# Kernel tuning notes

Measured on AMD Instinct MI355X. Metric: run time of the kernel, lower is better.

## Reference

```python
import jax, jax.numpy as jnp
import numpy as np

EPS = 1e-12  # torch F.normalize eps


def setup_inputs() -> dict:
    key = jax.random.key(0)
    ks = jax.random.split(key, 6)
    Bt, St, Bl, Sl, H, D = 128, 256, 128, 32, 768, 128
    return {
        "text_hidden": jax.random.normal(ks[0], (Bt, St, H), dtype=jnp.float32),
        "label_hidden": jax.random.normal(ks[1], (Bl, Sl, H), dtype=jnp.float32),
        "text_mask": jax.random.randint(ks[2], (Bt, St), 0, 2, dtype=jnp.int32),
        "label_mask": jax.random.randint(ks[3], (Bl, Sl), 0, 2, dtype=jnp.int32),
        "targets": jax.random.uniform(ks[4], (Bt, Bl), dtype=jnp.float32),
        "W_proj": jax.random.normal(ks[5], (H, D), dtype=jnp.float32) * (1.0 / np.sqrt(H)),
        "b_proj": jnp.zeros((D,), dtype=jnp.float32),
        "score_scale": jnp.asarray(10.0, dtype=jnp.float32),
    }


def _encode(hidden, W_proj, b_proj):
    # Linear projection + L2 normalize per token (torch F.normalize, eps=1e-12)
    p = hidden @ W_proj + b_proj  # [B, S, D]
    norm = jnp.maximum(jnp.linalg.norm(p, axis=-1, keepdims=True), EPS)
    return p / norm


def _maxsim(text_emb, text_mask, label_emb, label_mask):
    # all-pairs token similarity: [Bt, Bl, St, Sl]
    sim = jnp.einsum("tsd,lrd->tlsr", text_emb, label_emb)
    sim = jnp.where((text_mask == 0)[:, None, :, None], -jnp.inf, sim)
    max_sim = sim.max(axis=2)  # [Bt, Bl, Sl] max over text tokens
    max_sim = jnp.where((label_mask == 0)[None, :, :], 0.0, max_sim)
    label_lengths = jnp.clip(label_mask.sum(axis=-1), 1, None)[None, :]  # [1, Bl]
    return max_sim.sum(axis=-1) / label_lengths.astype(max_sim.dtype)  # [Bt, Bl]


def _bce_with_logits(logits, targets):
    # stable binary_cross_entropy_with_logits, mean reduction
    loss = jnp.maximum(logits, 0.0) - logits * targets + jnp.log1p(jnp.exp(-jnp.abs(logits)))
    return loss.mean()


def reference(text_hidden, label_hidden, text_mask, label_mask, targets, W_proj, b_proj, score_scale):
    text_emb = _encode(text_hidden, W_proj, b_proj)
    label_emb = _encode(label_hidden, W_proj, b_proj)
    logits = score_scale * _maxsim(text_emb, text_mask, label_emb, label_mask)
    loss = _bce_with_logits(logits, targets)
    return loss, jax.nn.sigmoid(logits)
```

## Files before the change

kernel.cpp:

```cpp
#include <hip/hip_runtime.h>
#include <hip/hip_bf16.h>
#include <math.h>

typedef __attribute__((ext_vector_type(8))) short short8;
typedef __attribute__((ext_vector_type(4))) float f32x4;

__device__ inline unsigned short f2bf(float x) {
    union { float f; unsigned u; } v; v.f = x;
    unsigned r = v.u + 0x7fff + ((v.u >> 16) & 1);
    return (unsigned short)(r >> 16);
}
__device__ inline float bf2f(unsigned short h) {
    union { unsigned u; float f; } v; v.u = ((unsigned)h) << 16;
    return v.f;
}

__global__ __launch_bounds__(256) void prep_w_kernel(
    const float* __restrict__ Wm, unsigned short* __restrict__ wfrag)
{
    const int g = blockIdx.x * 256 + threadIdx.x;
    const int c = g >> 10, s = g & 1023;
    const int rem = s & 511;
    const int l = rem & 63;
    const int n = ((rem >> 6) << 4) + (l & 15);
    const int k = c * 64 + ((s >> 9) << 5) + ((l >> 4) << 3);
    short8 hi, lo;
#pragma unroll
    for (int j = 0; j < 8; ++j) {
        const float wv = Wm[(size_t)(k + j) * 128 + n];
        const unsigned short h = f2bf(wv);
        hi[j] = (short)h;
        lo[j] = (short)f2bf(wv - bf2f(h));
    }
    *reinterpret_cast<short8*>(wfrag + (size_t)c * 16384 + s * 8) = hi;
    *reinterpret_cast<short8*>(wfrag + (size_t)c * 16384 + 8192 + s * 8) = lo;
}

__global__ __launch_bounds__(256, 2) void proj_mfma_kernel(
    const float* __restrict__ th, const float* __restrict__ lh,
    const unsigned short* __restrict__ wfrag, const float* __restrict__ bias,
    const int* __restrict__ tmask, const int* __restrict__ lmask,
    unsigned short* __restrict__ emb)
{
    __shared__ short lds[2][16384];
    const int tid = threadIdx.x;
    const int lane = tid & 63, w = tid >> 6;
    const int lq = lane >> 4, lr = lane & 15;
    const int rowg = blockIdx.x * 128;

    const float* sp; const int* mp;
    if (rowg < 32768) { sp = th + (size_t)rowg * 768; mp = tmask + rowg; }
    else { sp = lh + (size_t)(rowg - 32768) * 768; mp = lmask + (rowg - 32768); }

    const float* ap0 = sp + (size_t)(w * 32 + lr) * 768 + lq * 8;
    const float* ap1 = ap0 + (size_t)16 * 768;
    const short* wsrc = reinterpret_cast<const short*>(wfrag);

    f32x4 acc[2][8];
#pragma unroll
    for (int m = 0; m < 2; ++m)
#pragma unroll
        for (int n = 0; n < 8; ++n) acc[m][n] = (f32x4)(0.f);

    float bb[8];
#pragma unroll
    for (int n = 0; n < 8; ++n) bb[n] = bias[n * 16 + lr];

    short8 wst[8];
    f32x4 aA[8];

#pragma unroll
    for (int j = 0; j < 8; ++j)
        wst[j] = *reinterpret_cast<const short8*>(wsrc + (j * 256 + tid) * 8);
#pragma unroll
    for (int j = 0; j < 8; ++j)
        *reinterpret_cast<short8*>(&lds[0][(j * 256 + tid) * 8]) = wst[j];
#pragma unroll
    for (int m = 0; m < 2; ++m)
#pragma unroll
        for (int kcl = 0; kcl < 2; ++kcl)
#pragma unroll
            for (int h = 0; h < 2; ++h)
                aA[m * 4 + kcl * 2 + h] = *reinterpret_cast<const f32x4*>(
                    (m ? ap1 : ap0) + kcl * 32 + h * 4);
#pragma unroll
    for (int j = 0; j < 8; ++j)
        wst[j] = *reinterpret_cast<const short8*>(wsrc + 16384 + (j * 256 + tid) * 8);
    __syncthreads();

    for (int c = 0; c < 12; ++c) {
        const int cb = c & 1;
        short8 ah[2][2], al[2][2];
#pragma unroll
        for (int m = 0; m < 2; ++m)
#pragma unroll
            for (int kcl = 0; kcl < 2; ++kcl) {
                const f32x4 x0 = aA[m * 4 + kcl * 2], x1 = aA[m * 4 + kcl * 2 + 1];
#pragma unroll
                for (int j = 0; j < 8; ++j) {
                    const float av = (j < 4) ? x0[j] : x1[j - 4];
                    const unsigned short h = f2bf(av);
                    ah[m][kcl][j] = (short)h;
                    al[m][kcl][j] = (short)f2bf(av - bf2f(h));
                }
            }
        if (c < 11) {
#pragma unroll
            for (int m = 0; m < 2; ++m)
#pragma unroll
                for (int kcl = 0; kcl < 2; ++kcl)
#pragma unroll
                    for (int h = 0; h < 2; ++h)
                        aA[m * 4 + kcl * 2 + h] = *reinterpret_cast<const f32x4*>(
                            (m ? ap1 : ap0) + (c + 1) * 64 + kcl * 32 + h * 4);
        }
#pragma unroll
        for (int kcl = 0; kcl < 2; ++kcl) {
            short8 wf[8];
#pragma unroll
            for (int n = 0; n < 8; ++n)
                wf[n] = *reinterpret_cast<const short8*>(
                    &lds[cb][kcl * 4096 + n * 512 + lane * 8]);
#pragma unroll
            for (int m = 0; m < 2; ++m)
#pragma unroll
                for (int n = 0; n < 8; ++n)
                    acc[m][n] = __builtin_amdgcn_mfma_f32_16x16x32_bf16(
                        ah[m][kcl], wf[n], acc[m][n], 0, 0, 0);
#pragma unroll
            for (int m = 0; m < 2; ++m)
#pragma unroll
                for (int n = 0; n < 8; ++n)
                    acc[m][n] = __builtin_amdgcn_mfma_f32_16x16x32_bf16(
                        al[m][kcl], wf[n], acc[m][n], 0, 0, 0);
#pragma unroll
            for (int n = 0; n < 8; ++n)
                wf[n] = *reinterpret_cast<const short8*>(
                    &lds[cb][8192 + kcl * 4096 + n * 512 + lane * 8]);
#pragma unroll
            for (int m = 0; m < 2; ++m)
#pragma unroll
                for (int n = 0; n < 8; ++n)
                    acc[m][n] = __builtin_amdgcn_mfma_f32_16x16x32_bf16(
                        ah[m][kcl], wf[n], acc[m][n], 0, 0, 0);
        }
        if (c < 11) {
#pragma unroll
            for (int j = 0; j < 8; ++j)
                *reinterpret_cast<short8*>(&lds[cb ^ 1][(j * 256 + tid) * 8]) = wst[j];
        }
        if (c < 10) {
#pragma unroll
            for (int j = 0; j < 8; ++j)
                wst[j] = *reinterpret_cast<const short8*>(
                    wsrc + (size_t)(c + 2) * 16384 + (j * 256 + tid) * 8);
        }
        __syncthreads();
    }

#pragma unroll
    for (int m = 0; m < 2; ++m) {
#pragma unroll
        for (int n = 0; n < 8; ++n)
#pragma unroll
            for (int i2 = 0; i2 < 4; ++i2) acc[m][n][i2] += bb[n];
        float ss[4];
#pragma unroll
        for (int i2 = 0; i2 < 4; ++i2) {
            float s = 0.f;
#pragma unroll
            for (int n = 0; n < 8; ++n) s += acc[m][n][i2] * acc[m][n][i2];
            s += __shfl_xor(s, 1); s += __shfl_xor(s, 2);
            s += __shfl_xor(s, 4); s += __shfl_xor(s, 8);
            ss[i2] = s;
        }
#pragma unroll
        for (int i2 = 0; i2 < 4; ++i2) {
            const int rowl = w * 32 + m * 16 + lq * 4 + i2;
            float inv = 1.0f / fmaxf(sqrtf(ss[i2]), 1e-12f);
            if (mp[rowl] == 0) inv = 0.f;
#pragma unroll
            for (int n = 0; n < 8; ++n)
                emb[(size_t)(rowg + rowl) * 128 + n * 16 + lr] = f2bf(acc[m][n][i2] * inv);
        }
    }
}

__global__ __launch_bounds__(256, 2) void maxsim_kernel(
    const unsigned short* __restrict__ temb,
    const unsigned short* __restrict__ lemb,
    float* __restrict__ sums)
{
    const int t = blockIdx.x;
    const int bg = blockIdx.y;
    const int tid = threadIdx.x;
    const int lane = tid & 63, w = tid >> 6;
    const int lq = lane >> 4, lr = lane & 15;
    const short* tp = reinterpret_cast<const short*>(temb);
    const short* lp = reinterpret_cast<const short*>(lemb);
    const int l0 = bg * 16 + w * 4;

    short8 bfr[8][4];
#pragma unroll
    for (int n = 0; n < 8; ++n)
#pragma unroll
        for (int kc = 0; kc < 4; ++kc)
            bfr[n][kc] = *reinterpret_cast<const short8*>(
                lp + (size_t)(l0 * 32 + n * 16 + lr) * 128 + kc * 32 + lq * 8);

    f32x4 cmx[8];
#pragma unroll
    for (int n = 0; n < 8; ++n) cmx[n] = (f32x4)(-1e30f);

    const short* ap0 = tp + (size_t)(t * 256 + lr) * 128 + lq * 8;

    for (int m = 0; m < 16; ++m) {
        short8 afr[4];
#pragma unroll
        for (int kc = 0; kc < 4; ++kc)
            afr[kc] = *reinterpret_cast<const short8*>(ap0 + (size_t)m * 16 * 128 + kc * 32);
        f32x4 acc[8];
#pragma unroll
        for (int n = 0; n < 8; ++n) acc[n] = (f32x4)(0.f);
#pragma unroll
        for (int kc = 0; kc < 4; ++kc)
#pragma unroll
            for (int n = 0; n < 8; ++n)
                acc[n] = __builtin_amdgcn_mfma_f32_16x16x32_bf16(afr[kc], bfr[n][kc], acc[n], 0, 0, 0);
#pragma unroll
        for (int n = 0; n < 8; ++n) {
            cmx[n][0] = fmaxf(cmx[n][0], acc[n][0]);
            cmx[n][1] = fmaxf(cmx[n][1], acc[n][1]);
            cmx[n][2] = fmaxf(cmx[n][2], acc[n][2]);
            cmx[n][3] = fmaxf(cmx[n][3], acc[n][3]);
        }
    }

    float s[8];
#pragma unroll
    for (int n = 0; n < 8; ++n) {
        float v = fmaxf(fmaxf(cmx[n][0], cmx[n][1]), fmaxf(cmx[n][2], cmx[n][3]));
        v = fmaxf(v, __shfl_xor(v, 16));
        v = fmaxf(v, __shfl_xor(v, 32));
        v += __shfl_xor(v, 1);
        v += __shfl_xor(v, 2);
        v += __shfl_xor(v, 4);
        v += __shfl_xor(v, 8);
        s[n] = v;
    }
    if (lane == 0) {
#pragma unroll
        for (int li = 0; li < 4; ++li)
            sums[t * 128 + l0 + li] = s[2 * li] + s[2 * li + 1];
    }
}

__global__ __launch_bounds__(256) void finalize_kernel(
    const float* __restrict__ sums, const int* __restrict__ lmask,
    const float* __restrict__ targets, const float* __restrict__ scale_p,
    float* __restrict__ out)
{
    __shared__ float cl[128];
    const int tid = threadIdx.x;
    if (tid < 128) {
        int c = 0;
#pragma unroll
        for (int r = 0; r < 32; ++r) c += lmask[tid * 32 + r];
        cl[tid] = fmaxf((float)c, 1.0f);
    }
    __syncthreads();
    const float scale = *scale_p;
    float sum = 0.f;
    for (int i = tid; i < 16384; i += 256) {
        const float x = scale * sums[i] / cl[i & 127];
        const float tg = targets[i];
        out[1 + i] = 1.0f / (1.0f + expf(-x));
        sum += fmaxf(x, 0.f) - x * tg + log1pf(expf(-fabsf(x)));
    }
    __shared__ float part[4];
#pragma unroll
    for (int msk = 32; msk >= 1; msk >>= 1) sum += __shfl_xor(sum, msk);
    if ((tid & 63) == 0) part[tid >> 6] = sum;
    __syncthreads();
    if (tid == 0)
        out[0] = (part[0] + part[1] + part[2] + part[3]) * (1.0f / 16384.0f);
}

extern "C" void kernel_launch(void* const* d_in, const int* in_sizes, int n_in,
                              void* d_out, int out_size, void* d_ws, size_t ws_size,
                              hipStream_t stream) {
    const float* text_hidden  = (const float*)d_in[0];
    const float* label_hidden = (const float*)d_in[1];
    const int*   text_mask    = (const int*)d_in[2];
    const int*   label_mask   = (const int*)d_in[3];
    const float* targets      = (const float*)d_in[4];
    const float* W_proj       = (const float*)d_in[5];
    const float* b_proj       = (const float*)d_in[6];
    const float* score_scale  = (const float*)d_in[7];
    float* out = (float*)d_out;

    char* ws = (char*)d_ws;
    unsigned short* emb   = (unsigned short*)(ws);
    float*          sums  = (float*)(ws + 9437184);
    unsigned short* wfrag = (unsigned short*)(ws + 9502720);

    prep_w_kernel<<<48, 256, 0, stream>>>(W_proj, wfrag);
    proj_mfma_kernel<<<288, 256, 0, stream>>>(text_hidden, label_hidden, wfrag,
                                              b_proj, text_mask, label_mask, emb);
    maxsim_kernel<<<dim3(128, 8), 256, 0, stream>>>(emb, emb + (size_t)32768 * 128, sums);
    finalize_kernel<<<1, 256, 0, stream>>>(sums, label_mask, targets, score_scale, out);
}
```

Before: 297.9 us.

## Halve projection row tile and parallelize finalize across blocks

The projection kernel now handles 64 rows per block instead of 128, so it launches 576 blocks rather than 288 and spreads the work over more CUs. The cost is that each block reloads all of the W fragments for fewer rows and gets less reuse from its LDS tiles. The single-block finalize becomes a 64-block partial reduction followed by a small one-block sum kernel, which removes the serial loop but adds a kernel launch.

Result: faster. 250.4 us (-15.9%).

```diff
diff --git a/kernel.cpp b/kernel.cpp
--- a/kernel.cpp
+++ b/kernel.cpp
@@ -46,28 +46,25 @@
     const int tid = threadIdx.x;
     const int lane = tid & 63, w = tid >> 6;
     const int lq = lane >> 4, lr = lane & 15;
-    const int rowg = blockIdx.x * 128;
+    const int rowg = blockIdx.x * 64;
 
     const float* sp; const int* mp;
     if (rowg < 32768) { sp = th + (size_t)rowg * 768; mp = tmask + rowg; }
     else { sp = lh + (size_t)(rowg - 32768) * 768; mp = lmask + (rowg - 32768); }
 
-    const float* ap0 = sp + (size_t)(w * 32 + lr) * 768 + lq * 8;
-    const float* ap1 = ap0 + (size_t)16 * 768;
+    const float* ap = sp + (size_t)(w * 16 + lr) * 768 + lq * 8;
     const short* wsrc = reinterpret_cast<const short*>(wfrag);
 
-    f32x4 acc[2][8];
-#pragma unroll
-    for (int m = 0; m < 2; ++m)
-#pragma unroll
-        for (int n = 0; n < 8; ++n) acc[m][n] = (f32x4)(0.f);
+    f32x4 acc[8];
+#pragma unroll
+    for (int n = 0; n < 8; ++n) acc[n] = (f32x4)(0.f);
 
     float bb[8];
 #pragma unroll
     for (int n = 0; n < 8; ++n) bb[n] = bias[n * 16 + lr];
 
     short8 wst[8];
-    f32x4 aA[8];
+    f32x4 aA[4];
 
 #pragma unroll
     for (int j = 0; j < 8; ++j)
@@ -76,13 +73,10 @@
     for (int j = 0; j < 8; ++j)
         *reinterpret_cast<short8*>(&lds[0][(j * 256 + tid) * 8]) = wst[j];
 #pragma unroll
-    for (int m = 0; m < 2; ++m)
-#pragma unroll
-        for (int kcl = 0; kcl < 2; ++kcl)
-#pragma unroll
-            for (int h = 0; h < 2; ++h)
-                aA[m * 4 + kcl * 2 + h] = *reinterpret_cast<const f32x4*>(
-                    (m ? ap1 : ap0) + kcl * 32 + h * 4);
+    for (int kcl = 0; kcl < 2; ++kcl)
+#pragma unroll
+        for (int h = 0; h < 2; ++h)
+            aA[kcl * 2 + h] = *reinterpret_cast<const f32x4*>(ap + kcl * 32 + h * 4);
 #pragma unroll
     for (int j = 0; j < 8; ++j)
         wst[j] = *reinterpret_cast<const short8*>(wsrc + 16384 + (j * 256 + tid) * 8);
@@ -90,29 +84,25 @@
 
     for (int c = 0; c < 12; ++c) {
         const int cb = c & 1;
-        short8 ah[2][2], al[2][2];
-#pragma unroll
-        for (int m = 0; m < 2; ++m)
-#pragma unroll
-            for (int kcl = 0; kcl < 2; ++kcl) {
-                const f32x4 x0 = aA[m * 4 + kcl * 2], x1 = aA[m * 4 + kcl * 2 + 1];
-#pragma unroll
-                for (int j = 0; j < 8; ++j) {
-                    const float av = (j < 4) ? x0[j] : x1[j - 4];
-                    const unsigned short h = f2bf(av);
-                    ah[m][kcl][j] = (short)h;
-                    al[m][kcl][j] = (short)f2bf(av - bf2f(h));
-                }
+        short8 ah[2], al[2];
+#pragma unroll
+        for (int kcl = 0; kcl < 2; ++kcl) {
+            const f32x4 x0 = aA[kcl * 2], x1 = aA[kcl * 2 + 1];
+#pragma unroll
+            for (int j = 0; j < 8; ++j) {
+                const float av = (j < 4) ? x0[j] : x1[j - 4];
+                const unsigned short h = f2bf(av);
+                ah[kcl][j] = (short)h;
+                al[kcl][j] = (short)f2bf(av - bf2f(h));
             }
+        }
         if (c < 11) {
 #pragma unroll
-            for (int m = 0; m < 2; ++m)
-#pragma unroll
-                for (int kcl = 0; kcl < 2; ++kcl)
-#pragma unroll
-                    for (int h = 0; h < 2; ++h)
-                        aA[m * 4 + kcl * 2 + h] = *reinterpret_cast<const f32x4*>(
-                            (m ? ap1 : ap0) + (c + 1) * 64 + kcl * 32 + h * 4);
+            for (int kcl = 0; kcl < 2; ++kcl)
+#pragma unroll
+                for (int h = 0; h < 2; ++h)
+                    aA[kcl * 2 + h] = *reinterpret_cast<const f32x4*>(
+                        ap + (c + 1) * 64 + kcl * 32 + h * 4);
         }
 #pragma unroll
         for (int kcl = 0; kcl < 2; ++kcl) {
@@ -122,27 +112,18 @@
                 wf[n] = *reinterpret_cast<const short8*>(
                     &lds[cb][kcl * 4096 + n * 512 + lane * 8]);
 #pragma unroll
-            for (int m = 0; m < 2; ++m)
-#pragma unroll
-                for (int n = 0; n < 8; ++n)
-                    acc[m][n] = __builtin_amdgcn_mfma_f32_16x16x32_bf16(
-                        ah[m][kcl], wf[n], acc[m][n], 0, 0, 0);
-#pragma unroll
-            for (int m = 0; m < 2; ++m)
-#pragma unroll
-                for (int n = 0; n < 8; ++n)
-                    acc[m][n] = __builtin_amdgcn_mfma_f32_16x16x32_bf16(
-                        al[m][kcl], wf[n], acc[m][n], 0, 0, 0);
+            for (int n = 0; n < 8; ++n)
+                acc[n] = __builtin_amdgcn_mfma_f32_16x16x32_bf16(ah[kcl], wf[n], acc[n], 0, 0, 0);
+#pragma unroll
+            for (int n = 0; n < 8; ++n)
+                acc[n] = __builtin_amdgcn_mfma_f32_16x16x32_bf16(al[kcl], wf[n], acc[n], 0, 0, 0);
 #pragma unroll
             for (int n = 0; n < 8; ++n)
                 wf[n] = *reinterpret_cast<const short8*>(
                     &lds[cb][8192 + kcl * 4096 + n * 512 + lane * 8]);
 #pragma unroll
-            for (int m = 0; m < 2; ++m)
-#pragma unroll
-                for (int n = 0; n < 8; ++n)
-                    acc[m][n] = __builtin_amdgcn_mfma_f32_16x16x32_bf16(
-                        ah[m][kcl], wf[n], acc[m][n], 0, 0, 0);
+            for (int n = 0; n < 8; ++n)
+                acc[n] = __builtin_amdgcn_mfma_f32_16x16x32_bf16(ah[kcl], wf[n], acc[n], 0, 0, 0);
         }
         if (c < 11) {
 #pragma unroll
@@ -159,30 +140,27 @@
     }
 
 #pragma unroll
-    for (int m = 0; m < 2; ++m) {
+    for (int n = 0; n < 8; ++n)
+#pragma unroll
+        for (int i2 = 0; i2 < 4; ++i2) acc[n][i2] += bb[n];
+    float ss[4];
+#pragma unroll
+    for (int i2 = 0; i2 < 4; ++i2) {
+        float s = 0.f;
+#pragma unroll
+        for (int n = 0; n < 8; ++n) s += acc[n][i2] * acc[n][i2];
+        s += __shfl_xor(s, 1); s += __shfl_xor(s, 2);
+        s += __shfl_xor(s, 4); s += __shfl_xor(s, 8);
+        ss[i2] = s;
+    }
+#pragma unroll
+    for (int i2 = 0; i2 < 4; ++i2) {
+        const int rowl = w * 16 + lq * 4 + i2;
+        float inv = 1.0f / fmaxf(sqrtf(ss[i2]), 1e-12f);
+        if (mp[rowl] == 0) inv = 0.f;
 #pragma unroll
         for (int n = 0; n < 8; ++n)
-#pragma unroll
-            for (int i2 = 0; i2 < 4; ++i2) acc[m][n][i2] += bb[n];
-        float ss[4];
-#pragma unroll
-        for (int i2 = 0; i2 < 4; ++i2) {
-            float s = 0.f;
-#pragma unroll
-            for (int n = 0; n < 8; ++n) s += acc[m][n][i2] * acc[m][n][i2];
-            s += __shfl_xor(s, 1); s += __shfl_xor(s, 2);
-            s += __shfl_xor(s, 4); s += __shfl_xor(s, 8);
-            ss[i2] = s;
-        }
-#pragma unroll
-        for (int i2 = 0; i2 < 4; ++i2) {
-            const int rowl = w * 32 + m * 16 + lq * 4 + i2;
-            float inv = 1.0f / fmaxf(sqrtf(ss[i2]), 1e-12f);
-            if (mp[rowl] == 0) inv = 0.f;
-#pragma unroll
-            for (int n = 0; n < 8; ++n)
-                emb[(size_t)(rowg + rowl) * 128 + n * 16 + lr] = f2bf(acc[m][n][i2] * inv);
-        }
+            emb[(size_t)(rowg + rowl) * 128 + n * 16 + lr] = f2bf(acc[n][i2] * inv);
     }
 }
 
@@ -255,10 +233,10 @@
     }
 }
 
-__global__ __launch_bounds__(256) void finalize_kernel(
+__global__ __launch_bounds__(256) void finalize_part(
     const float* __restrict__ sums, const int* __restrict__ lmask,
     const float* __restrict__ targets, const float* __restrict__ scale_p,
-    float* __restrict__ out)
+    float* __restrict__ out, float* __restrict__ partials)
 {
     __shared__ float cl[128];
     const int tid = threadIdx.x;
@@ -270,20 +248,26 @@
     }
     __syncthreads();
     const float scale = *scale_p;
-    float sum = 0.f;
-    for (int i = tid; i < 16384; i += 256) {
-        const float x = scale * sums[i] / cl[i & 127];
-        const float tg = targets[i];
-        out[1 + i] = 1.0f / (1.0f + expf(-x));
-        sum += fmaxf(x, 0.f) - x * tg + log1pf(expf(-fabsf(x)));
-    }
+    const int i = blockIdx.x * 256 + tid;
+    const float x = scale * sums[i] / cl[i & 127];
+    const float tg = targets[i];
+    out[1 + i] = 1.0f / (1.0f + expf(-x));
+    float sum = fmaxf(x, 0.f) - x * tg + log1pf(expf(-fabsf(x)));
+#pragma unroll
+    for (int msk = 32; msk >= 1; msk >>= 1) sum += __shfl_xor(sum, msk);
     __shared__ float part[4];
-#pragma unroll
-    for (int msk = 32; msk >= 1; msk >>= 1) sum += __shfl_xor(sum, msk);
     if ((tid & 63) == 0) part[tid >> 6] = sum;
     __syncthreads();
     if (tid == 0)
-        out[0] = (part[0] + part[1] + part[2] + part[3]) * (1.0f / 16384.0f);
+        partials[blockIdx.x] = part[0] + part[1] + part[2] + part[3];
+}
+
+__global__ void finalize_sum(const float* __restrict__ partials, float* __restrict__ out)
+{
+    float v = partials[threadIdx.x];
+#pragma unroll
+    for (int msk = 32; msk >= 1; msk >>= 1) v += __shfl_xor(v, msk);
+    if (threadIdx.x == 0) out[0] = v * (1.0f / 16384.0f);
 }
 
 extern "C" void kernel_launch(void* const* d_in, const int* in_sizes, int n_in,
@@ -300,13 +284,16 @@
     float* out = (float*)d_out;
 
     char* ws = (char*)d_ws;
-    unsigned short* emb   = (unsigned short*)(ws);
-    float*          sums  = (float*)(ws + 9437184);
-    unsigned short* wfrag = (unsigned short*)(ws + 9502720);
+    unsigned short* emb      = (unsigned short*)(ws);
+    float*          sums     = (float*)(ws + 9437184);
+    unsigned short* wfrag    = (unsigned short*)(ws + 9502720);
+    float*          partials = (float*)(ws + 9895936);
 
     prep_w_kernel<<<48, 256, 0, stream>>>(W_proj, wfrag);
-    proj_mfma_kernel<<<288, 256, 0, stream>>>(text_hidden, label_hidden, wfrag,
+    proj_mfma_kernel<<<576, 256, 0, stream>>>(text_hidden, label_hidden, wfrag,
                                               b_proj, text_mask, label_mask, emb);
     maxsim_kernel<<<dim3(128, 8), 256, 0, stream>>>(emb, emb + (size_t)32768 * 128, sums);
-    finalize_kernel<<<1, 256, 0, stream>>>(sums, label_mask, targets, score_scale, out);
-}
+    finalize_part<<<64, 256, 0, stream>>>(sums, label_mask, targets, score_scale,
+                                          out, partials);
+    finalize_sum<<<1, 64, 0, stream>>>(partials, out);
+}
```
